# Kernel tuning notes

Hardware: AMD Instinct MI355X
Metric: run time of the kernel (lower is better)

Reference implementation:

```python
import jax, jax.numpy as jnp
import numpy as np

B, D, H = 512, 512, 512  # batch, input dim, hidden dim


def setup_inputs() -> dict:
    key = jax.random.key(0)
    ks = jax.random.split(key, 7)
    s = 1.0 / np.sqrt(D)
    return {
        "x": jax.random.normal(ks[0], (B, D), jnp.float32),
        "W1": jax.random.normal(ks[1], (D, H), jnp.float32) * s,
        "b1": jax.random.normal(ks[2], (H,), jnp.float32) * 0.01,
        "W2": jax.random.normal(ks[3], (H, H), jnp.float32) * s,
        "b2": jax.random.normal(ks[4], (H,), jnp.float32) * 0.01,
        "w3": jax.random.normal(ks[5], (H,), jnp.float32) * s,
        "b3": jax.random.normal(ks[6], (1,), jnp.float32) * 0.01,
    }


def _per_sample(xi, W1, b1, W2, b2, w3, b3):
    # Sequential layers applied to one sample; per-sample scalar loss.
    h = jax.nn.relu(xi @ W1 + b1)
    h = jax.nn.relu(h @ W2 + b2)
    return h @ w3 + b3[0]


def reference(x, W1, b1, W2, b2, w3, b3):
    # Forward pass (vectorized over the batch) -> per-sample losses [B].
    h = jax.nn.relu(x @ W1 + b1)
    h = jax.nn.relu(h @ W2 + b2)
    output = h @ w3 + b3[0]  # [B]

    # _autogram: per-sample Jacobian w.r.t. all layer parameters with a seed
    # of ones (grad = ones_like(output)); gramian accumulates J @ J.T per
    # parameter block. jax.vmap(jax.grad) == torch.vmap(vjp) with scalar seed 1.
    grad_fn = jax.grad(_per_sample, argnums=(1, 2, 3, 4, 5, 6))
    grads = jax.vmap(grad_fn, in_axes=(0, None, None, None, None, None, None))(
        x, W1, b1, W2, b2, w3, b3
    )  # pytree of per-sample grads, each leaf [B, *param_shape]

    bsz = x.shape[0]
    gramian = jnp.zeros((bsz, bsz), x.dtype)
    for g in grads:  # fixed small number of parameter tensors (matches per-layer loop)
        J = g.reshape(bsz, -1)  # [B, n_params_block]
        gramian = gramian + J @ J.T
    return output, gramian
```

## Files before the change

### kernel.cpp

```cpp
#include <hip/hip_runtime.h>


#define NN 512

typedef __attribute__((ext_vector_type(8))) short v8s;
typedef __attribute__((ext_vector_type(4))) float v4f;

static __device__ __forceinline__ unsigned short f2bf(float f) {
    union { float f; unsigned u; } v; v.f = f;
    unsigned r = v.u + 0x7FFF + ((v.u >> 16) & 1);
    return (unsigned short)(r >> 16);
}
static __device__ __forceinline__ float bf2f(unsigned short h) {
    union { unsigned u; float f; } v; v.u = ((unsigned)h) << 16;
    return v.f;
}

#define MFMA(a, b, c) __builtin_amdgcn_mfma_f32_16x16x32_bf16(a, b, c, 0, 0, 0)

__global__ __launch_bounds__(256) void prep(
    const float* __restrict__ x, const float* __restrict__ W1,
    const float* __restrict__ W2, const float* __restrict__ b3,
    unsigned short* __restrict__ xhi, unsigned short* __restrict__ xlo,
    unsigned short* __restrict__ W1th, unsigned short* __restrict__ W1tl,
    unsigned short* __restrict__ W2th, unsigned short* __restrict__ W2tl,
    unsigned short* __restrict__ W2b, float* __restrict__ out) {
    __shared__ float T[32][33];
    const int t = threadIdx.x;
    const int lr = t >> 3, lc = (t & 7) * 4;
    const int r0 = blockIdx.y * 32, c0 = blockIdx.x * 32;
    const int z = blockIdx.z;
    if (z == 2) {
        float4 v = *(const float4*)&x[(r0 + lr) * NN + c0 + lc];
        ushort4 hi, lo;
        hi.x = f2bf(v.x); lo.x = f2bf(v.x - bf2f(hi.x));
        hi.y = f2bf(v.y); lo.y = f2bf(v.y - bf2f(hi.y));
        hi.z = f2bf(v.z); lo.z = f2bf(v.z - bf2f(hi.z));
        hi.w = f2bf(v.w); lo.w = f2bf(v.w - bf2f(hi.w));
        *(ushort4*)&xhi[(r0 + lr) * NN + c0 + lc] = hi;
        *(ushort4*)&xlo[(r0 + lr) * NN + c0 + lc] = lo;
        if (blockIdx.x == 0 && t < 32) out[r0 + t] = b3[0];
        return;
    }
    const float* src = (z == 1) ? W2 : W1;
    float4 v = *(const float4*)&src[(r0 + lr) * NN + c0 + lc];
    if (z == 1) {
        ushort4 h;
        h.x = f2bf(v.x); h.y = f2bf(v.y); h.z = f2bf(v.z); h.w = f2bf(v.w);
        *(ushort4*)&W2b[(r0 + lr) * NN + c0 + lc] = h;
    }
    T[lr][lc + 0] = v.x; T[lr][lc + 1] = v.y;
    T[lr][lc + 2] = v.z; T[lr][lc + 3] = v.w;
    __syncthreads();
    unsigned short* dh = (z == 1) ? W2th : W1th;
    unsigned short* dl = (z == 1) ? W2tl : W1tl;
    float a0 = T[lc + 0][lr], a1 = T[lc + 1][lr];
    float a2 = T[lc + 2][lr], a3 = T[lc + 3][lr];
    ushort4 hi, lo;
    hi.x = f2bf(a0); lo.x = f2bf(a0 - bf2f(hi.x));
    hi.y = f2bf(a1); lo.y = f2bf(a1 - bf2f(hi.y));
    hi.z = f2bf(a2); lo.z = f2bf(a2 - bf2f(hi.z));
    hi.w = f2bf(a3); lo.w = f2bf(a3 - bf2f(hi.w));
    *(ushort4*)&dh[(c0 + lr) * NN + r0 + lc] = hi;
    *(ushort4*)&dl[(c0 + lr) * NN + r0 + lc] = lo;
}

__global__ __launch_bounds__(1024, 4) void fwd1(
    const unsigned short* __restrict__ Ahi, const unsigned short* __restrict__ Alo,
    const unsigned short* __restrict__ Bhi, const unsigned short* __restrict__ Blo,
    const float* __restrict__ bias,
    unsigned short* __restrict__ Chi, unsigned short* __restrict__ Clo) {
    __shared__ float red[12][64][4];
    const int t = threadIdx.x;
    const int wave = t >> 6, lane = t & 63;
    const int q = wave & 3, s = wave >> 2;
    const int r = lane & 15, quad = lane >> 4;
    const int i0 = blockIdx.y * 32 + 16 * (q >> 1);
    const int j0 = blockIdx.x * 32 + 16 * (q & 1);
    const int ao = (i0 + r) * NN + quad * 8 + s * 128;
    const int bo = (j0 + r) * NN + quad * 8 + s * 128;
    v4f hh = {0.f, 0.f, 0.f, 0.f}, lh = hh, hl = hh;
    #pragma unroll
    for (int k0 = 0; k0 < 128; k0 += 32) {
        v8s ah = *(const v8s*)(Ahi + ao + k0);
        v8s al = *(const v8s*)(Alo + ao + k0);
        v8s bh = *(const v8s*)(Bhi + bo + k0);
        v8s bl = *(const v8s*)(Blo + bo + k0);
        hh = MFMA(ah, bh, hh);
        lh = MFMA(al, bh, lh);
        hl = MFMA(ah, bl, hl);
    }
    v4f z;
    #pragma unroll
    for (int rr = 0; rr < 4; ++rr) z[rr] = (hh[rr] + lh[rr]) + hl[rr];
    if (s > 0) *(v4f*)red[(s - 1) * 4 + q][lane] = z;
    __syncthreads();
    if (s == 0) {
        v4f z0 = z + *(v4f*)red[q][lane] + *(v4f*)red[4 + q][lane]
                   + *(v4f*)red[8 + q][lane];
        const float bj = bias[j0 + r];
        #pragma unroll
        for (int rr = 0; rr < 4; ++rr) {
            const int i = i0 + quad * 4 + rr, j = j0 + r;
            float zv = z0[rr] + bj;
            float h = zv > 0.f ? zv : 0.f;
            unsigned short hi = f2bf(h);
            Chi[i * NN + j] = hi;
            Clo[i * NN + j] = f2bf(h - bf2f(hi));
        }
    }
}

__global__ __launch_bounds__(1024, 4) void fwd2(
    const unsigned short* __restrict__ Ahi, const unsigned short* __restrict__ Alo,
    const unsigned short* __restrict__ Bhi, const unsigned short* __restrict__ Blo,
    const float* __restrict__ b2, const float* __restrict__ w3,
    unsigned short* __restrict__ H2b, unsigned short* __restrict__ G2b,
    float* __restrict__ out) {
    __shared__ float red[12][64][4];
    const int t = threadIdx.x;
    const int wave = t >> 6, lane = t & 63;
    const int q = wave & 3, s = wave >> 2;
    const int r = lane & 15, quad = lane >> 4;
    const int i0 = blockIdx.y * 32 + 16 * (q >> 1);
    const int j0 = blockIdx.x * 32 + 16 * (q & 1);
    const int ao = (i0 + r) * NN + quad * 8 + s * 128;
    const int bo = (j0 + r) * NN + quad * 8 + s * 128;
    v4f hh = {0.f, 0.f, 0.f, 0.f}, lh = hh, hl = hh;
    #pragma unroll
    for (int k0 = 0; k0 < 128; k0 += 32) {
        v8s ah = *(const v8s*)(Ahi + ao + k0);
        v8s al = *(const v8s*)(Alo + ao + k0);
        v8s bh = *(const v8s*)(Bhi + bo + k0);
        v8s bl = *(const v8s*)(Blo + bo + k0);
        hh = MFMA(ah, bh, hh);
        lh = MFMA(al, bh, lh);
        hl = MFMA(ah, bl, hl);
    }
    v4f z;
    #pragma unroll
    for (int rr = 0; rr < 4; ++rr) z[rr] = (hh[rr] + lh[rr]) + hl[rr];
    if (s > 0) *(v4f*)red[(s - 1) * 4 + q][lane] = z;
    __syncthreads();
    if (s == 0) {
        v4f z0 = z + *(v4f*)red[q][lane] + *(v4f*)red[4 + q][lane]
                   + *(v4f*)red[8 + q][lane];
        const float bj = b2[j0 + r];
        const float wj = w3[j0 + r];
        const unsigned short wjb = f2bf(wj);
        #pragma unroll
        for (int rr = 0; rr < 4; ++rr) {
            const int i = i0 + quad * 4 + rr, j = j0 + r;
            float zv = z0[rr] + bj;
            float h = zv > 0.f ? zv : 0.f;
            H2b[i * NN + j] = f2bf(h);
            G2b[i * NN + j] = (zv > 0.f) ? wjb : (unsigned short)0;
            float p = h * wj;
            p += __shfl_xor(p, 1, 64);
            p += __shfl_xor(p, 2, 64);
            p += __shfl_xor(p, 4, 64);
            p += __shfl_xor(p, 8, 64);
            if (r == 0) atomicAdd(&out[i], p);
        }
    }
}

__global__ __launch_bounds__(1024, 4) void g1k(
    const unsigned short* __restrict__ G2b, const unsigned short* __restrict__ W2b,
    const unsigned short* __restrict__ H1b, unsigned short* __restrict__ G1b) {
    __shared__ float red[12][64][4];
    const int t = threadIdx.x;
    const int wave = t >> 6, lane = t & 63;
    const int q = wave & 3, s = wave >> 2;
    const int r = lane & 15, quad = lane >> 4;
    const int i0 = blockIdx.y * 32 + 16 * (q >> 1);
    const int c0 = blockIdx.x * 32 + 16 * (q & 1);
    const unsigned short* arow = G2b + (i0 + r) * NN + quad * 8 + s * 128;
    const unsigned short* brow = W2b + (c0 + r) * NN + quad * 8 + s * 128;
    v4f acc = {0.f, 0.f, 0.f, 0.f};
    #pragma unroll
    for (int k0 = 0; k0 < 128; k0 += 32) {
        v8s a = *(const v8s*)(arow + k0);
        v8s b = *(const v8s*)(brow + k0);
        acc = MFMA(a, b, acc);
    }
    if (s > 0) *(v4f*)red[(s - 1) * 4 + q][lane] = acc;
    __syncthreads();
    if (s == 0) {
        v4f a0 = acc + *(v4f*)red[q][lane] + *(v4f*)red[4 + q][lane]
                     + *(v4f*)red[8 + q][lane];
        #pragma unroll
        for (int rr = 0; rr < 4; ++rr) {
            const int i = i0 + quad * 4 + rr;
            const int c = c0 + r;
            float v = (H1b[i * NN + c] != 0) ? a0[rr] : 0.f;
            G1b[i * NN + c] = f2bf(v);
        }
    }
}

__global__ __launch_bounds__(1024, 4) void gramk(
    const unsigned short* __restrict__ Xb, const unsigned short* __restrict__ H1b,
    const unsigned short* __restrict__ G1b, const unsigned short* __restrict__ H2b,
    const unsigned short* __restrict__ G2b, float* __restrict__ gram) {
    __shared__ float red[12][64][5][4];
    const int t = threadIdx.x;
    const int wave = t >> 6, lane = t & 63;
    const int q = wave & 3, s = wave >> 2;
    const int r = lane & 15, quad = lane >> 4;
    const int i0 = blockIdx.y * 32 + 16 * (q >> 1);
    const int j0 = blockIdx.x * 32 + 16 * (q & 1);
    const int ao = (i0 + r) * NN + quad * 8 + s * 128;
    const int bo = (j0 + r) * NN + quad * 8 + s * 128;
    v4f a0 = {0.f, 0.f, 0.f, 0.f}, a1 = a0, a2 = a0, a3 = a0, a4 = a0;
    #pragma unroll
    for (int k0 = 0; k0 < 128; k0 += 32) {
        v8s xa = *(const v8s*)(Xb  + ao + k0), xb2 = *(const v8s*)(Xb  + bo + k0);
        v8s ha = *(const v8s*)(H1b + ao + k0), hb  = *(const v8s*)(H1b + bo + k0);
        v8s ga = *(const v8s*)(G1b + ao + k0), gb  = *(const v8s*)(G1b + bo + k0);
        v8s ua = *(const v8s*)(H2b + ao + k0), ub  = *(const v8s*)(H2b + bo + k0);
        v8s va = *(const v8s*)(G2b + ao + k0), vb  = *(const v8s*)(G2b + bo + k0);
        a0 = MFMA(xa, xb2, a0);
        a1 = MFMA(ha, hb,  a1);
        a2 = MFMA(ga, gb,  a2);
        a3 = MFMA(ua, ub,  a3);
        a4 = MFMA(va, vb,  a4);
    }
    if (s > 0) {
        const int idx = (s - 1) * 4 + q;
        *(v4f*)red[idx][lane][0] = a0;
        *(v4f*)red[idx][lane][1] = a1;
        *(v4f*)red[idx][lane][2] = a2;
        *(v4f*)red[idx][lane][3] = a3;
        *(v4f*)red[idx][lane][4] = a4;
    }
    __syncthreads();
    if (s == 0) {
        #pragma unroll
        for (int u = 0; u < 3; ++u) {
            const int idx = u * 4 + q;
            a0 += *(v4f*)red[idx][lane][0];
            a1 += *(v4f*)red[idx][lane][1];
            a2 += *(v4f*)red[idx][lane][2];
            a3 += *(v4f*)red[idx][lane][3];
            a4 += *(v4f*)red[idx][lane][4];
        }
        #pragma unroll
        for (int rr = 0; rr < 4; ++rr) {
            const int i = i0 + quad * 4 + rr;
            const int j = j0 + r;
            float g = 1.f + a3[rr] + a4[rr] * (1.f + a1[rr]) + a2[rr] * (1.f + a0[rr]);
            gram[i * NN + j] = g;
        }
    }
}

extern "C" void kernel_launch(void* const* d_in, const int* in_sizes, int n_in,
                              void* d_out, int out_size, void* d_ws, size_t ws_size,
                              hipStream_t stream) {
    const float* x  = (const float*)d_in[0];
    const float* W1 = (const float*)d_in[1];
    const float* b1 = (const float*)d_in[2];
    const float* W2 = (const float*)d_in[3];
    const float* b2 = (const float*)d_in[4];
    const float* w3 = (const float*)d_in[5];
    const float* b3 = (const float*)d_in[6];

    float* out  = (float*)d_out;
    float* gram = out + NN;

    unsigned short* p    = (unsigned short*)d_ws;
    unsigned short* xhi  = p;  p += NN * NN;
    unsigned short* xlo  = p;  p += NN * NN;
    unsigned short* W1th = p;  p += NN * NN;
    unsigned short* W1tl = p;  p += NN * NN;
    unsigned short* W2th = p;  p += NN * NN;
    unsigned short* W2tl = p;  p += NN * NN;
    unsigned short* W2b  = p;  p += NN * NN;
    unsigned short* H1b  = p;  p += NN * NN;
    unsigned short* H1lo = p;  p += NN * NN;
    unsigned short* H2b  = p;  p += NN * NN;
    unsigned short* G2b  = p;  p += NN * NN;
    unsigned short* G1b  = p;  p += NN * NN;

    dim3 blk(256);
    dim3 big(1024);
    prep <<<dim3(16, 16, 3), blk, 0, stream>>>(x, W1, W2, b3, xhi, xlo,
                                               W1th, W1tl, W2th, W2tl, W2b, out);
    fwd1 <<<dim3(16, 16), big, 0, stream>>>(xhi, xlo, W1th, W1tl, b1, H1b, H1lo);
    fwd2 <<<dim3(16, 16), big, 0, stream>>>(H1b, H1lo, W2th, W2tl, b2, w3,
                                            H2b, G2b, out);
    g1k  <<<dim3(16, 16), big, 0, stream>>>(G2b, W2b, H1b, G1b);
    gramk<<<dim3(16, 16), big, 0, stream>>>(xhi, H1b, G1b, H2b, G2b, gram);
}
```

Baseline: 116.0 us.

## Fuse fwd1, fwd2 and g1k into one row-chain kernel with LDS-resident activations

Replaces three separate 16x16-grid kernels (layer1 forward, layer2 forward, layer1 gradient) with one kernel where each block owns 16 batch rows and keeps H1 hi/lo, H2 and G2 in swizzled shared memory between stages. This removes two launches and the global round-trips of the intermediates, and drops the H1lo workspace buffer. In exchange, only 32 blocks run, each wave doing the full K=512 reduction serially, so most CUs sit idle and per-block latency grows.

```diff
diff --git a/kernel.cpp b/kernel.cpp
--- a/kernel.cpp
+++ b/kernel.cpp
@@ -65,137 +65,131 @@
     *(ushort4*)&dl[(c0 + lr) * NN + r0 + lc] = lo;
 }
 
-__global__ __launch_bounds__(1024, 4) void fwd1(
-    const unsigned short* __restrict__ Ahi, const unsigned short* __restrict__ Alo,
-    const unsigned short* __restrict__ Bhi, const unsigned short* __restrict__ Blo,
-    const float* __restrict__ bias,
-    unsigned short* __restrict__ Chi, unsigned short* __restrict__ Clo) {
-    __shared__ float red[12][64][4];
+__global__ __launch_bounds__(1024, 1) void rowchain(
+    const unsigned short* __restrict__ xhi, const unsigned short* __restrict__ xlo,
+    const unsigned short* __restrict__ W1th, const unsigned short* __restrict__ W1tl,
+    const unsigned short* __restrict__ W2th, const unsigned short* __restrict__ W2tl,
+    const unsigned short* __restrict__ W2b,
+    const float* __restrict__ b1, const float* __restrict__ b2,
+    const float* __restrict__ w3,
+    unsigned short* __restrict__ H1b, unsigned short* __restrict__ H2b,
+    unsigned short* __restrict__ G2b, unsigned short* __restrict__ G1b,
+    float* __restrict__ out) {
+    __shared__ unsigned short Hhi[16][512];
+    __shared__ unsigned short Hlo[16][512];
+    __shared__ unsigned short H2s[16][512];
+    __shared__ unsigned short G2s[16][512];
     const int t = threadIdx.x;
     const int wave = t >> 6, lane = t & 63;
-    const int q = wave & 3, s = wave >> 2;
     const int r = lane & 15, quad = lane >> 4;
-    const int i0 = blockIdx.y * 32 + 16 * (q >> 1);
-    const int j0 = blockIdx.x * 32 + 16 * (q & 1);
-    const int ao = (i0 + r) * NN + quad * 8 + s * 128;
-    const int bo = (j0 + r) * NN + quad * 8 + s * 128;
-    v4f hh = {0.f, 0.f, 0.f, 0.f}, lh = hh, hl = hh;
+    const int i0 = blockIdx.x * 16;
+    const int j0 = wave * 32;
+    const int ao = (i0 + r) * NN + quad * 8;
+
+    for (int jt = 0; jt < 32; jt += 16) {
+        const int bo = (j0 + jt + r) * NN + quad * 8;
+        v4f hh = {0.f, 0.f, 0.f, 0.f}, lh = hh, hl = hh;
+        #pragma unroll
+        for (int k0 = 0; k0 < NN; k0 += 32) {
+            v8s ah = *(const v8s*)(xhi + ao + k0);
+            v8s al = *(const v8s*)(xlo + ao + k0);
+            v8s bh = *(const v8s*)(W1th + bo + k0);
+            v8s bl = *(const v8s*)(W1tl + bo + k0);
+            hh = MFMA(ah, bh, hh);
+            lh = MFMA(al, bh, lh);
+            hl = MFMA(ah, bl, hl);
+        }
+        const int j = j0 + jt + r;
+        const float bj = b1[j];
+        #pragma unroll
+        for (int rr = 0; rr < 4; ++rr) {
+            const int row = quad * 4 + rr;
+            float zv = (hh[rr] + lh[rr]) + hl[rr] + bj;
+            float h = zv > 0.f ? zv : 0.f;
+            unsigned short hb = f2bf(h);
+            const int cb = (2 * j) ^ ((row & 7) << 4);
+            *(unsigned short*)((char*)Hhi + row * 1024 + cb) = hb;
+            *(unsigned short*)((char*)Hlo + row * 1024 + cb) = f2bf(h - bf2f(hb));
+        }
+    }
+    __syncthreads();
+    {
+        const int row = wave;
+        const int cb = (lane * 16) ^ ((row & 7) << 4);
+        v8s vv = *(const v8s*)((char*)Hhi + row * 1024 + cb);
+        *(v8s*)(H1b + (i0 + row) * NN + lane * 8) = vv;
+    }
+
+    float psum[4] = {0.f, 0.f, 0.f, 0.f};
+    for (int jt = 0; jt < 32; jt += 16) {
+        const int bo = (j0 + jt + r) * NN + quad * 8;
+        v4f hh = {0.f, 0.f, 0.f, 0.f}, lh = hh, hl = hh;
+        #pragma unroll
+        for (int k0 = 0; k0 < NN; k0 += 32) {
+            const int cb = (2 * (k0 + quad * 8)) ^ ((r & 7) << 4);
+            v8s ah = *(const v8s*)((char*)Hhi + r * 1024 + cb);
+            v8s al = *(const v8s*)((char*)Hlo + r * 1024 + cb);
+            v8s bh = *(const v8s*)(W2th + bo + k0);
+            v8s bl = *(const v8s*)(W2tl + bo + k0);
+            hh = MFMA(ah, bh, hh);
+            lh = MFMA(al, bh, lh);
+            hl = MFMA(ah, bl, hl);
+        }
+        const int j = j0 + jt + r;
+        const float bj = b2[j];
+        const float wj = w3[j];
+        const unsigned short wjb = f2bf(wj);
+        #pragma unroll
+        for (int rr = 0; rr < 4; ++rr) {
+            const int row = quad * 4 + rr;
+            float zv = (hh[rr] + lh[rr]) + hl[rr] + bj;
+            float h = zv > 0.f ? zv : 0.f;
+            const int cb = (2 * j) ^ ((row & 7) << 4);
+            *(unsigned short*)((char*)H2s + row * 1024 + cb) = f2bf(h);
+            *(unsigned short*)((char*)G2s + row * 1024 + cb) =
+                (zv > 0.f) ? wjb : (unsigned short)0;
+            psum[rr] += h * wj;
+        }
+    }
     #pragma unroll
-    for (int k0 = 0; k0 < 128; k0 += 32) {
-        v8s ah = *(const v8s*)(Ahi + ao + k0);
-        v8s al = *(const v8s*)(Alo + ao + k0);
-        v8s bh = *(const v8s*)(Bhi + bo + k0);
-        v8s bl = *(const v8s*)(Blo + bo + k0);
-        hh = MFMA(ah, bh, hh);
-        lh = MFMA(al, bh, lh);
-        hl = MFMA(ah, bl, hl);
-    }
-    v4f z;
-    #pragma unroll
-    for (int rr = 0; rr < 4; ++rr) z[rr] = (hh[rr] + lh[rr]) + hl[rr];
-    if (s > 0) *(v4f*)red[(s - 1) * 4 + q][lane] = z;
-    __syncthreads();
-    if (s == 0) {
-        v4f z0 = z + *(v4f*)red[q][lane] + *(v4f*)red[4 + q][lane]
-                   + *(v4f*)red[8 + q][lane];
-        const float bj = bias[j0 + r];
-        #pragma unroll
-        for (int rr = 0; rr < 4; ++rr) {
-            const int i = i0 + quad * 4 + rr, j = j0 + r;
-            float zv = z0[rr] + bj;
-            float h = zv > 0.f ? zv : 0.f;
-            unsigned short hi = f2bf(h);
-            Chi[i * NN + j] = hi;
-            Clo[i * NN + j] = f2bf(h - bf2f(hi));
-        }
-    }
-}
-
-__global__ __launch_bounds__(1024, 4) void fwd2(
-    const unsigned short* __restrict__ Ahi, const unsigned short* __restrict__ Alo,
-    const unsigned short* __restrict__ Bhi, const unsigned short* __restrict__ Blo,
-    const float* __restrict__ b2, const float* __restrict__ w3,
-    unsigned short* __restrict__ H2b, unsigned short* __restrict__ G2b,
-    float* __restrict__ out) {
-    __shared__ float red[12][64][4];
-    const int t = threadIdx.x;
-    const int wave = t >> 6, lane = t & 63;
-    const int q = wave & 3, s = wave >> 2;
-    const int r = lane & 15, quad = lane >> 4;
-    const int i0 = blockIdx.y * 32 + 16 * (q >> 1);
-    const int j0 = blockIdx.x * 32 + 16 * (q & 1);
-    const int ao = (i0 + r) * NN + quad * 8 + s * 128;
-    const int bo = (j0 + r) * NN + quad * 8 + s * 128;
-    v4f hh = {0.f, 0.f, 0.f, 0.f}, lh = hh, hl = hh;
-    #pragma unroll
-    for (int k0 = 0; k0 < 128; k0 += 32) {
-        v8s ah = *(const v8s*)(Ahi + ao + k0);
-        v8s al = *(const v8s*)(Alo + ao + k0);
-        v8s bh = *(const v8s*)(Bhi + bo + k0);
-        v8s bl = *(const v8s*)(Blo + bo + k0);
-        hh = MFMA(ah, bh, hh);
-        lh = MFMA(al, bh, lh);
-        hl = MFMA(ah, bl, hl);
-    }
-    v4f z;
-    #pragma unroll
-    for (int rr = 0; rr < 4; ++rr) z[rr] = (hh[rr] + lh[rr]) + hl[rr];
-    if (s > 0) *(v4f*)red[(s - 1) * 4 + q][lane] = z;
-    __syncthreads();
-    if (s == 0) {
-        v4f z0 = z + *(v4f*)red[q][lane] + *(v4f*)red[4 + q][lane]
-                   + *(v4f*)red[8 + q][lane];
-        const float bj = b2[j0 + r];
-        const float wj = w3[j0 + r];
-        const unsigned short wjb = f2bf(wj);
-        #pragma unroll
-        for (int rr = 0; rr < 4; ++rr) {
-            const int i = i0 + quad * 4 + rr, j = j0 + r;
-            float zv = z0[rr] + bj;
-            float h = zv > 0.f ? zv : 0.f;
-            H2b[i * NN + j] = f2bf(h);
-            G2b[i * NN + j] = (zv > 0.f) ? wjb : (unsigned short)0;
-            float p = h * wj;
-            p += __shfl_xor(p, 1, 64);
-            p += __shfl_xor(p, 2, 64);
-            p += __shfl_xor(p, 4, 64);
-            p += __shfl_xor(p, 8, 64);
-            if (r == 0) atomicAdd(&out[i], p);
-        }
-    }
-}
-
-__global__ __launch_bounds__(1024, 4) void g1k(
-    const unsigned short* __restrict__ G2b, const unsigned short* __restrict__ W2b,
-    const unsigned short* __restrict__ H1b, unsigned short* __restrict__ G1b) {
-    __shared__ float red[12][64][4];
-    const int t = threadIdx.x;
-    const int wave = t >> 6, lane = t & 63;
-    const int q = wave & 3, s = wave >> 2;
-    const int r = lane & 15, quad = lane >> 4;
-    const int i0 = blockIdx.y * 32 + 16 * (q >> 1);
-    const int c0 = blockIdx.x * 32 + 16 * (q & 1);
-    const unsigned short* arow = G2b + (i0 + r) * NN + quad * 8 + s * 128;
-    const unsigned short* brow = W2b + (c0 + r) * NN + quad * 8 + s * 128;
-    v4f acc = {0.f, 0.f, 0.f, 0.f};
-    #pragma unroll
-    for (int k0 = 0; k0 < 128; k0 += 32) {
-        v8s a = *(const v8s*)(arow + k0);
-        v8s b = *(const v8s*)(brow + k0);
-        acc = MFMA(a, b, acc);
-    }
-    if (s > 0) *(v4f*)red[(s - 1) * 4 + q][lane] = acc;
-    __syncthreads();
-    if (s == 0) {
-        v4f a0 = acc + *(v4f*)red[q][lane] + *(v4f*)red[4 + q][lane]
-                     + *(v4f*)red[8 + q][lane];
-        #pragma unroll
-        for (int rr = 0; rr < 4; ++rr) {
-            const int i = i0 + quad * 4 + rr;
-            const int c = c0 + r;
-            float v = (H1b[i * NN + c] != 0) ? a0[rr] : 0.f;
-            G1b[i * NN + c] = f2bf(v);
-        }
+    for (int rr = 0; rr < 4; ++rr) {
+        float p = psum[rr];
+        p += __shfl_xor(p, 1, 64);
+        p += __shfl_xor(p, 2, 64);
+        p += __shfl_xor(p, 4, 64);
+        p += __shfl_xor(p, 8, 64);
+        if (r == 0) atomicAdd(&out[i0 + quad * 4 + rr], p);
+    }
+    __syncthreads();
+
+    for (int ct = 0; ct < 32; ct += 16) {
+        const int bo = (j0 + ct + r) * NN + quad * 8;
+        v4f acc = {0.f, 0.f, 0.f, 0.f};
+        #pragma unroll
+        for (int k0 = 0; k0 < NN; k0 += 32) {
+            const int cb = (2 * (k0 + quad * 8)) ^ ((r & 7) << 4);
+            v8s a = *(const v8s*)((char*)G2s + r * 1024 + cb);
+            v8s b = *(const v8s*)(W2b + bo + k0);
+            acc = MFMA(a, b, acc);
+        }
+        const int c = j0 + ct + r;
+        #pragma unroll
+        for (int rr = 0; rr < 4; ++rr) {
+            const int row = quad * 4 + rr;
+            const int cb = (2 * c) ^ ((row & 7) << 4);
+            unsigned short m = *(const unsigned short*)((char*)Hhi + row * 1024 + cb);
+            float v = (m != 0) ? acc[rr] : 0.f;
+            *(unsigned short*)((char*)Hlo + row * 1024 + cb) = f2bf(v);
+        }
+    }
+    __syncthreads();
+    {
+        const int row = wave;
+        const int cb = (lane * 16) ^ ((row & 7) << 4);
+        const int go = (i0 + row) * NN + lane * 8;
+        *(v8s*)(H2b + go) = *(const v8s*)((char*)H2s + row * 1024 + cb);
+        *(v8s*)(G2b + go) = *(const v8s*)((char*)G2s + row * 1024 + cb);
+        *(v8s*)(G1b + go) = *(const v8s*)((char*)Hlo + row * 1024 + cb);
     }
 }
 
@@ -278,18 +272,15 @@
     unsigned short* W2tl = p;  p += NN * NN;
     unsigned short* W2b  = p;  p += NN * NN;
     unsigned short* H1b  = p;  p += NN * NN;
-    unsigned short* H1lo = p;  p += NN * NN;
     unsigned short* H2b  = p;  p += NN * NN;
     unsigned short* G2b  = p;  p += NN * NN;
     unsigned short* G1b  = p;  p += NN * NN;
 
-    dim3 blk(256);
-    dim3 big(1024);
-    prep <<<dim3(16, 16, 3), blk, 0, stream>>>(x, W1, W2, b3, xhi, xlo,
-                                               W1th, W1tl, W2th, W2tl, W2b, out);
-    fwd1 <<<dim3(16, 16), big, 0, stream>>>(xhi, xlo, W1th, W1tl, b1, H1b, H1lo);
-    fwd2 <<<dim3(16, 16), big, 0, stream>>>(H1b, H1lo, W2th, W2tl, b2, w3,
-                                            H2b, G2b, out);
-    g1k  <<<dim3(16, 16), big, 0, stream>>>(G2b, W2b, H1b, G1b);
-    gramk<<<dim3(16, 16), big, 0, stream>>>(xhi, H1b, G1b, H2b, G2b, gram);
-}
+    prep <<<dim3(16, 16, 3), dim3(256), 0, stream>>>(
+        x, W1, W2, b3, xhi, xlo, W1th, W1tl, W2th, W2tl, W2b, out);
+    rowchain<<<dim3(32), dim3(1024), 0, stream>>>(
+        xhi, xlo, W1th, W1tl, W2th, W2tl, W2b, b1, b2, w3,
+        H1b, H2b, G2b, G1b, out);
+    gramk<<<dim3(16, 16), dim3(1024), 0, stream>>>(
+        xhi, H1b, G1b, H2b, G2b, gram);
+}
```

Measured after the change: 189.1 us. +63.0%, slower.

## Split gramian products across earlier kernels to shorten the critical path

Applied to the files above, without the earlier changes.

Moves the x·xᵀ gramian term into an extra z-slice of the first forward kernel, and the H1/H2/G2 gramian terms into an extra z-slice of the G1 backprop kernel. The final gram kernel then only computes G1·G1ᵀ and combines it with the fp32 partials. Each launch now has more independent blocks to fill the GPU, and the last kernel does less serial work. In exchange, two fp32 NxN intermediates are written and read back through the workspace.

```diff
diff --git a/kernel.cpp b/kernel.cpp
--- a/kernel.cpp
+++ b/kernel.cpp
@@ -65,11 +65,12 @@
     *(ushort4*)&dl[(c0 + lr) * NN + r0 + lc] = lo;
 }
 
-__global__ __launch_bounds__(1024, 4) void fwd1(
+__global__ __launch_bounds__(1024, 4) void fwd1x(
     const unsigned short* __restrict__ Ahi, const unsigned short* __restrict__ Alo,
     const unsigned short* __restrict__ Bhi, const unsigned short* __restrict__ Blo,
     const float* __restrict__ bias,
-    unsigned short* __restrict__ Chi, unsigned short* __restrict__ Clo) {
+    unsigned short* __restrict__ Chi, unsigned short* __restrict__ Clo,
+    float* __restrict__ SXX) {
     __shared__ float red[12][64][4];
     const int t = threadIdx.x;
     const int wave = t >> 6, lane = t & 63;
@@ -79,6 +80,25 @@
     const int j0 = blockIdx.x * 32 + 16 * (q & 1);
     const int ao = (i0 + r) * NN + quad * 8 + s * 128;
     const int bo = (j0 + r) * NN + quad * 8 + s * 128;
+    if (blockIdx.z == 1) {
+        v4f acc = {0.f, 0.f, 0.f, 0.f};
+        #pragma unroll
+        for (int k0 = 0; k0 < 128; k0 += 32) {
+            v8s a = *(const v8s*)(Ahi + ao + k0);
+            v8s b = *(const v8s*)(Ahi + bo + k0);
+            acc = MFMA(a, b, acc);
+        }
+        if (s > 0) *(v4f*)red[(s - 1) * 4 + q][lane] = acc;
+        __syncthreads();
+        if (s == 0) {
+            v4f a0 = acc + *(v4f*)red[q][lane] + *(v4f*)red[4 + q][lane]
+                         + *(v4f*)red[8 + q][lane];
+            #pragma unroll
+            for (int rr = 0; rr < 4; ++rr)
+                SXX[(i0 + quad * 4 + rr) * NN + j0 + r] = a0[rr];
+        }
+        return;
+    }
     v4f hh = {0.f, 0.f, 0.f, 0.f}, lh = hh, hl = hh;
     #pragma unroll
     for (int k0 = 0; k0 < 128; k0 += 32) {
@@ -165,45 +185,11 @@
     }
 }
 
-__global__ __launch_bounds__(1024, 4) void g1k(
+__global__ __launch_bounds__(1024, 4) void g1p(
     const unsigned short* __restrict__ G2b, const unsigned short* __restrict__ W2b,
-    const unsigned short* __restrict__ H1b, unsigned short* __restrict__ G1b) {
-    __shared__ float red[12][64][4];
-    const int t = threadIdx.x;
-    const int wave = t >> 6, lane = t & 63;
-    const int q = wave & 3, s = wave >> 2;
-    const int r = lane & 15, quad = lane >> 4;
-    const int i0 = blockIdx.y * 32 + 16 * (q >> 1);
-    const int c0 = blockIdx.x * 32 + 16 * (q & 1);
-    const unsigned short* arow = G2b + (i0 + r) * NN + quad * 8 + s * 128;
-    const unsigned short* brow = W2b + (c0 + r) * NN + quad * 8 + s * 128;
-    v4f acc = {0.f, 0.f, 0.f, 0.f};
-    #pragma unroll
-    for (int k0 = 0; k0 < 128; k0 += 32) {
-        v8s a = *(const v8s*)(arow + k0);
-        v8s b = *(const v8s*)(brow + k0);
-        acc = MFMA(a, b, acc);
-    }
-    if (s > 0) *(v4f*)red[(s - 1) * 4 + q][lane] = acc;
-    __syncthreads();
-    if (s == 0) {
-        v4f a0 = acc + *(v4f*)red[q][lane] + *(v4f*)red[4 + q][lane]
-                     + *(v4f*)red[8 + q][lane];
-        #pragma unroll
-        for (int rr = 0; rr < 4; ++rr) {
-            const int i = i0 + quad * 4 + rr;
-            const int c = c0 + r;
-            float v = (H1b[i * NN + c] != 0) ? a0[rr] : 0.f;
-            G1b[i * NN + c] = f2bf(v);
-        }
-    }
-}
-
-__global__ __launch_bounds__(1024, 4) void gramk(
-    const unsigned short* __restrict__ Xb, const unsigned short* __restrict__ H1b,
-    const unsigned short* __restrict__ G1b, const unsigned short* __restrict__ H2b,
-    const unsigned short* __restrict__ G2b, float* __restrict__ gram) {
-    __shared__ float red[12][64][5][4];
+    const unsigned short* __restrict__ H1b, const unsigned short* __restrict__ H2b,
+    unsigned short* __restrict__ G1b, float* __restrict__ P) {
+    __shared__ float red[12][64][3][4];
     const int t = threadIdx.x;
     const int wave = t >> 6, lane = t & 63;
     const int q = wave & 3, s = wave >> 2;
@@ -212,45 +198,90 @@
     const int j0 = blockIdx.x * 32 + 16 * (q & 1);
     const int ao = (i0 + r) * NN + quad * 8 + s * 128;
     const int bo = (j0 + r) * NN + quad * 8 + s * 128;
-    v4f a0 = {0.f, 0.f, 0.f, 0.f}, a1 = a0, a2 = a0, a3 = a0, a4 = a0;
+    if (blockIdx.z == 1) {
+        v4f a1 = {0.f, 0.f, 0.f, 0.f}, a3 = a1, a4 = a1;
+        #pragma unroll
+        for (int k0 = 0; k0 < 128; k0 += 32) {
+            v8s ha = *(const v8s*)(H1b + ao + k0), hb = *(const v8s*)(H1b + bo + k0);
+            v8s ua = *(const v8s*)(H2b + ao + k0), ub = *(const v8s*)(H2b + bo + k0);
+            v8s va = *(const v8s*)(G2b + ao + k0), vb = *(const v8s*)(G2b + bo + k0);
+            a1 = MFMA(ha, hb, a1);
+            a3 = MFMA(ua, ub, a3);
+            a4 = MFMA(va, vb, a4);
+        }
+        if (s > 0) {
+            const int idx = (s - 1) * 4 + q;
+            *(v4f*)red[idx][lane][0] = a1;
+            *(v4f*)red[idx][lane][1] = a3;
+            *(v4f*)red[idx][lane][2] = a4;
+        }
+        __syncthreads();
+        if (s == 0) {
+            #pragma unroll
+            for (int u = 0; u < 3; ++u) {
+                const int idx = u * 4 + q;
+                a1 += *(v4f*)red[idx][lane][0];
+                a3 += *(v4f*)red[idx][lane][1];
+                a4 += *(v4f*)red[idx][lane][2];
+            }
+            #pragma unroll
+            for (int rr = 0; rr < 4; ++rr) {
+                const int i = i0 + quad * 4 + rr, j = j0 + r;
+                P[i * NN + j] = a3[rr] + a4[rr] * (1.f + a1[rr]);
+            }
+        }
+        return;
+    }
+    v4f acc = {0.f, 0.f, 0.f, 0.f};
     #pragma unroll
     for (int k0 = 0; k0 < 128; k0 += 32) {
-        v8s xa = *(const v8s*)(Xb  + ao + k0), xb2 = *(const v8s*)(Xb  + bo + k0);
-        v8s ha = *(const v8s*)(H1b + ao + k0), hb  = *(const v8s*)(H1b + bo + k0);
-        v8s ga = *(const v8s*)(G1b + ao + k0), gb  = *(const v8s*)(G1b + bo + k0);
-        v8s ua = *(const v8s*)(H2b + ao + k0), ub  = *(const v8s*)(H2b + bo + k0);
-        v8s va = *(const v8s*)(G2b + ao + k0), vb  = *(const v8s*)(G2b + bo + k0);
-        a0 = MFMA(xa, xb2, a0);
-        a1 = MFMA(ha, hb,  a1);
-        a2 = MFMA(ga, gb,  a2);
-        a3 = MFMA(ua, ub,  a3);
-        a4 = MFMA(va, vb,  a4);
-    }
-    if (s > 0) {
-        const int idx = (s - 1) * 4 + q;
-        *(v4f*)red[idx][lane][0] = a0;
-        *(v4f*)red[idx][lane][1] = a1;
-        *(v4f*)red[idx][lane][2] = a2;
-        *(v4f*)red[idx][lane][3] = a3;
-        *(v4f*)red[idx][lane][4] = a4;
-    }
+        v8s a = *(const v8s*)(G2b + ao + k0);
+        v8s b = *(const v8s*)(W2b + bo + k0);
+        acc = MFMA(a, b, acc);
+    }
+    if (s > 0) *(v4f*)red[(s - 1) * 4 + q][lane][0] = acc;
     __syncthreads();
     if (s == 0) {
-        #pragma unroll
-        for (int u = 0; u < 3; ++u) {
-            const int idx = u * 4 + q;
-            a0 += *(v4f*)red[idx][lane][0];
-            a1 += *(v4f*)red[idx][lane][1];
-            a2 += *(v4f*)red[idx][lane][2];
-            a3 += *(v4f*)red[idx][lane][3];
-            a4 += *(v4f*)red[idx][lane][4];
-        }
+        v4f a0 = acc + *(v4f*)red[q][lane][0] + *(v4f*)red[4 + q][lane][0]
+                     + *(v4f*)red[8 + q][lane][0];
         #pragma unroll
         for (int rr = 0; rr < 4; ++rr) {
             const int i = i0 + quad * 4 + rr;
-            const int j = j0 + r;
-            float g = 1.f + a3[rr] + a4[rr] * (1.f + a1[rr]) + a2[rr] * (1.f + a0[rr]);
-            gram[i * NN + j] = g;
+            const int c = j0 + r;
+            float v = (H1b[i * NN + c] != 0) ? a0[rr] : 0.f;
+            G1b[i * NN + c] = f2bf(v);
+        }
+    }
+}
+
+__global__ __launch_bounds__(1024, 4) void gramf(
+    const unsigned short* __restrict__ G1b, const float* __restrict__ SXX,
+    const float* __restrict__ P, float* __restrict__ gram) {
+    __shared__ float red[12][64][4];
+    const int t = threadIdx.x;
+    const int wave = t >> 6, lane = t & 63;
+    const int q = wave & 3, s = wave >> 2;
+    const int r = lane & 15, quad = lane >> 4;
+    const int i0 = blockIdx.y * 32 + 16 * (q >> 1);
+    const int j0 = blockIdx.x * 32 + 16 * (q & 1);
+    const int ao = (i0 + r) * NN + quad * 8 + s * 128;
+    const int bo = (j0 + r) * NN + quad * 8 + s * 128;
+    v4f acc = {0.f, 0.f, 0.f, 0.f};
+    #pragma unroll
+    for (int k0 = 0; k0 < 128; k0 += 32) {
+        v8s a = *(const v8s*)(G1b + ao + k0);
+        v8s b = *(const v8s*)(G1b + bo + k0);
+        acc = MFMA(a, b, acc);
+    }
+    if (s > 0) *(v4f*)red[(s - 1) * 4 + q][lane] = acc;
+    __syncthreads();
+    if (s == 0) {
+        v4f a2 = acc + *(v4f*)red[q][lane] + *(v4f*)red[4 + q][lane]
+                     + *(v4f*)red[8 + q][lane];
+        #pragma unroll
+        for (int rr = 0; rr < 4; ++rr) {
+            const int i = i0 + quad * 4 + rr, j = j0 + r;
+            gram[i * NN + j] = 1.f + P[i * NN + j] + a2[rr] * (1.f + SXX[i * NN + j]);
         }
     }
 }
@@ -282,14 +313,17 @@
     unsigned short* H2b  = p;  p += NN * NN;
     unsigned short* G2b  = p;  p += NN * NN;
     unsigned short* G1b  = p;  p += NN * NN;
-
-    dim3 blk(256);
-    dim3 big(1024);
-    prep <<<dim3(16, 16, 3), blk, 0, stream>>>(x, W1, W2, b3, xhi, xlo,
-                                               W1th, W1tl, W2th, W2tl, W2b, out);
-    fwd1 <<<dim3(16, 16), big, 0, stream>>>(xhi, xlo, W1th, W1tl, b1, H1b, H1lo);
-    fwd2 <<<dim3(16, 16), big, 0, stream>>>(H1b, H1lo, W2th, W2tl, b2, w3,
-                                            H2b, G2b, out);
-    g1k  <<<dim3(16, 16), big, 0, stream>>>(G2b, W2b, H1b, G1b);
-    gramk<<<dim3(16, 16), big, 0, stream>>>(xhi, H1b, G1b, H2b, G2b, gram);
-}
+    float* SXX = (float*)p;  p += 2 * NN * NN;
+    float* Pf  = (float*)p;  p += 2 * NN * NN;
+
+    prep <<<dim3(16, 16, 3), dim3(256), 0, stream>>>(
+        x, W1, W2, b3, xhi, xlo, W1th, W1tl, W2th, W2tl, W2b, out);
+    fwd1x<<<dim3(16, 16, 2), dim3(1024), 0, stream>>>(
+        xhi, xlo, W1th, W1tl, b1, H1b, H1lo, SXX);
+    fwd2 <<<dim3(16, 16), dim3(1024), 0, stream>>>(
+        H1b, H1lo, W2th, W2tl, b2, w3, H2b, G2b, out);
+    g1p  <<<dim3(16, 16, 2), dim3(1024), 0, stream>>>(
+        G2b, W2b, H1b, H2b, G1b, Pf);
+    gramf<<<dim3(16, 16), dim3(1024), 0, stream>>>(
+        G1b, SXX, Pf, gram);
+}
```

Result: no change. 115.8 us (-0.1%).
